# Kernel optimization log

Hardware: AMD Instinct MI355X
Metric: run time of the kernel (lower is better)

Reference implementation:

```python
import jax, jax.numpy as jnp
import numpy as np

N, E, D, R = 8192, 131072, 128, 32
SIZES = (3, 5, 7)  # per-degree component counts (2l+1)
LN_EPS = 1e-5


def setup_inputs() -> dict:
    key = jax.random.key(0)
    ks = jax.random.split(key, 20)
    rn = lambda k, shape, s=1.0: jax.random.normal(k, shape, jnp.float32) * s
    inp = {
        'X0': rn(ks[0], (N, SIZES[0], D)),
        'X1': rn(ks[1], (N, SIZES[1], D)),
        'X2': rn(ks[2], (N, SIZES[2], D)),
        't_ij': rn(ks[3], (E, D)),
        'r0': rn(ks[4], (E, SIZES[0])),
        'r1': rn(ks[5], (E, SIZES[1])),
        'r2': rn(ks[6], (E, SIZES[2])),
        'edge_index': jax.random.randint(ks[7], (2, E), 0, N, dtype=jnp.int32),
        # params
        'W_vq': rn(ks[8], (D, R), D ** -0.5),
        'W_vk0': rn(ks[9], (D, R), D ** -0.5),
        'W_vk1': rn(ks[10], (D, R), D ** -0.5),
        'W_vk2': rn(ks[11], (D, R), D ** -0.5),
        'ln_g': jnp.ones((R,), jnp.float32),
        'ln_b': jnp.zeros((R,), jnp.float32),
        'W_w': rn(ks[12], (R, D), R ** -0.5),
        'b_w': jnp.zeros((D,), jnp.float32),
        'W_t1': rn(ks[13], (D, D), D ** -0.5),
        'b_t1': jnp.zeros((D,), jnp.float32),
        'W_t2': rn(ks[14], (D, D), D ** -0.5),
        'b_t2': jnp.zeros((D,), jnp.float32),
    }
    return inp


def _vec_rej(x, r):
    # x: [E, L, R], r: [E, L]; dot over component dim (L), keepdim, subtract projection
    r = r[..., None]
    dot = jnp.sum(x * r, axis=1, keepdims=True)  # [E, 1, R]
    return x - dot * r


def reference(X0, X1, X2, t_ij, r0, r1, r2, edge_index,
              W_vq, W_vk0, W_vk1, W_vk2, ln_g, ln_b, W_w, b_w,
              W_t1, b_t1, W_t2, b_t2):
    n_j, n_i = edge_index[0], edge_index[1]
    X_ls = jnp.concatenate([X0, X1, X2], axis=1)                 # [N, 15, D]
    eq_i = jnp.einsum('nld,dr->nlr', X_ls, W_vq)[n_i]            # [E, 15, R]
    ek = jnp.concatenate([
        jnp.einsum('nld,dr->nlr', X0, W_vk0),
        jnp.einsum('nld,dr->nlr', X1, W_vk1),
        jnp.einsum('nld,dr->nlr', X2, W_vk2)], axis=1)
    ek_j = ek[n_j]                                               # [E, 15, R]
    # per-degree vector rejection (vec_rej=True)
    qs, ksl, off = [], [], 0
    for r in (r0, r1, r2):
        s = r.shape[1]
        qs.append(_vec_rej(eq_i[:, off:off + s], r))
        ksl.append(_vec_rej(ek_j[:, off:off + s], -r))
        off += s
    eq_i = jnp.concatenate(qs, axis=1)
    ek_j = jnp.concatenate(ksl, axis=1)
    w_ij = jnp.sum(eq_i * ek_j, axis=1)                          # [E, R]
    # mlp_w = LayerNorm + Linear
    mu = jnp.mean(w_ij, axis=-1, keepdims=True)
    var = jnp.var(w_ij, axis=-1, keepdims=True)
    wn = (w_ij - mu) * jax.lax.rsqrt(var + LN_EPS) * ln_g + ln_b
    dw = wn @ W_w + b_w                                          # [E, D]
    # mlp_t = Linear -> silu -> Linear, then outer activation
    t = jax.nn.silu(t_ij @ W_t1 + b_t1) @ W_t2 + b_t2            # [E, D]
    return dw * jax.nn.silu(t)
```

## Files before the change

### kernel.cpp

```cpp
#include <hip/hip_runtime.h>
#include <hip/hip_bf16.h>

#define N_NODES 8192
#define N_EDGES 131072
#define LN_EPS  1e-5f

typedef __attribute__((ext_vector_type(8))) short bf16x8;
typedef __attribute__((ext_vector_type(4))) float f32x4;

__device__ __forceinline__ float silu_f(float x) {
    return x / (1.0f + __expf(-x));
}

__device__ __forceinline__ unsigned short f2bf(float x) {
    union { float f; unsigned int u; } v; v.f = x;
    unsigned int r = v.u + 0x7FFFu + ((v.u >> 16) & 1u);
    return (unsigned short)(r >> 16);
}
__device__ __forceinline__ float bf2f(unsigned short u) {
    union { float f; unsigned int x; } v; v.x = ((unsigned int)u) << 16;
    return v.f;
}
__device__ __forceinline__ unsigned int pk2(float a, float b) {
    float2 t; t.x = a; t.y = b;
    union { __hip_bfloat162 h; unsigned int u; } v;
    v.h = __float22bfloat162_rn(t);
    return v.u;
}
__device__ __forceinline__ bf16x8 pack8(float4 u, float4 v) {
    union { bf16x8 b; unsigned int w[4]; } o;
    o.w[0] = pk2(u.x, u.y); o.w[1] = pk2(u.z, u.w);
    o.w[2] = pk2(v.x, v.y); o.w[3] = pk2(v.z, v.w);
    return o.b;
}
__device__ __forceinline__ f32x4 mfma16(bf16x8 a, bf16x8 b, f32x4 c) {
    return __builtin_amdgcn_mfma_f32_16x16x32_bf16(a, b, c, 0, 0, 0);
}

__global__ __launch_bounds__(256) void prep_kernel(
    const float* __restrict__ W_w, const float* __restrict__ W_t1,
    const float* __restrict__ W_t2, const float* __restrict__ Wvq,
    const float* __restrict__ Wvk0, const float* __restrict__ Wvk1,
    const float* __restrict__ Wvk2,
    unsigned short* __restrict__ Wtw, unsigned short* __restrict__ Wt1b,
    unsigned short* __restrict__ Wt2b, unsigned short* __restrict__ Wqt,
    unsigned short* __restrict__ Wk0t, unsigned short* __restrict__ Wk1t,
    unsigned short* __restrict__ Wk2t)
{
    int i = blockIdx.x * 256 + threadIdx.x;
    if (i < 16384) {
        int n = i >> 7, k = i & 127;
        Wt1b[i] = f2bf(W_t1[k * 128 + n]);
        Wt2b[i] = f2bf(W_t2[k * 128 + n]);
    }
    if (i < 4096) {
        { int n = i >> 5, k = i & 31; Wtw[i] = f2bf(W_w[k * 128 + n]); }
        int r = i >> 7, d = i & 127;
        Wqt[i]  = f2bf(Wvq [d * 32 + r]);
        Wk0t[i] = f2bf(Wvk0[d * 32 + r]);
        Wk1t[i] = f2bf(Wvk1[d * 32 + r]);
        Wk2t[i] = f2bf(Wvk2[d * 32 + r]);
    }
}

template<int S, int LOFF>
__device__ __forceinline__ void proj_body(
    const float* __restrict__ X, const unsigned short* __restrict__ Wqt,
    const unsigned short* __restrict__ Wkt,
    unsigned short* __restrict__ eq, unsigned short* __restrict__ ek,
    int row0)
{
    const int tid  = threadIdx.x;
    const int lane = tid & 63;
    const int wv   = tid >> 6;
    const int l15  = lane & 15;
    const int lk   = lane >> 4;
    const int xrow = row0 + wv * 16 + l15;

    bf16x8 xf[4];
    #pragma unroll
    for (int kt = 0; kt < 4; ++kt) {
        const float* p = X + (size_t)xrow * 128 + kt * 32 + lk * 8;
        xf[kt] = pack8(*(const float4*)p, *(const float4*)(p + 4));
    }

    f32x4 qa[2], ka[2];
    #pragma unroll
    for (int h = 0; h < 2; ++h) {
        qa[h] = (f32x4){0.f, 0.f, 0.f, 0.f};
        ka[h] = (f32x4){0.f, 0.f, 0.f, 0.f};
    }
    #pragma unroll
    for (int kt = 0; kt < 4; ++kt) {
        #pragma unroll
        for (int h = 0; h < 2; ++h) {
            bf16x8 wq = *(const bf16x8*)&Wqt[(h * 16 + l15) * 128 + kt * 32 + lk * 8];
            bf16x8 wk = *(const bf16x8*)&Wkt[(h * 16 + l15) * 128 + kt * 32 + lk * 8];
            qa[h] = mfma16(wq, xf[kt], qa[h]);
            ka[h] = mfma16(wk, xf[kt], ka[h]);
        }
    }

    const int n = xrow / S;
    const int l = xrow % S + LOFF;
    const size_t base = (size_t)n * 480 + (size_t)l * 32;
    #pragma unroll
    for (int h = 0; h < 2; ++h) {
        int rb = h * 16 + lk * 4;
        union { ushort4 s; unsigned int u[2]; } pq, pk_;
        pq.u[0]  = pk2(qa[h][0], qa[h][1]); pq.u[1]  = pk2(qa[h][2], qa[h][3]);
        pk_.u[0] = pk2(ka[h][0], ka[h][1]); pk_.u[1] = pk2(ka[h][2], ka[h][3]);
        *(ushort4*)&eq[base + rb] = pq.s;
        *(ushort4*)&ek[base + rb] = pk_.s;
    }
}

__global__ __launch_bounds__(256) void proj_kernel(
    const float* __restrict__ X0, const float* __restrict__ X1,
    const float* __restrict__ X2,
    const unsigned short* __restrict__ Wqt,
    const unsigned short* __restrict__ Wk0t,
    const unsigned short* __restrict__ Wk1t,
    const unsigned short* __restrict__ Wk2t,
    unsigned short* __restrict__ eq, unsigned short* __restrict__ ek)
{
    const int b = blockIdx.x;
    if (b < 384)
        proj_body<3, 0>(X0, Wqt, Wk0t, eq, ek, b * 64);
    else if (b < 1024)
        proj_body<5, 3>(X1, Wqt, Wk1t, eq, ek, (b - 384) * 64);
    else
        proj_body<7, 8>(X2, Wqt, Wk2t, eq, ek, (b - 1024) * 64);
}

__global__ __launch_bounds__(256) void wn_kernel(
    const unsigned short* __restrict__ eq, const unsigned short* __restrict__ ek,
    const float* __restrict__ r0, const float* __restrict__ r1,
    const float* __restrict__ r2, const int* __restrict__ eidx,
    const float* __restrict__ ln_g, const float* __restrict__ ln_b,
    unsigned short* __restrict__ wn)
{
    const int tid = threadIdx.x;
    const int r   = tid & 31;
    const int e   = blockIdx.x * 8 + (tid >> 5);
    const float g  = ln_g[r];
    const float bb = ln_b[r];
    const int nj = eidx[e];
    const int ni = eidx[N_EDGES + e];

    float q[15], k[15], rv[15];
    const unsigned short* qp = eq + (size_t)ni * 480 + r;
    const unsigned short* kp = ek + (size_t)nj * 480 + r;
    #pragma unroll
    for (int l = 0; l < 15; ++l) { q[l] = bf2f(qp[l * 32]); k[l] = bf2f(kp[l * 32]); }
    #pragma unroll
    for (int c = 0; c < 3; ++c) rv[c]     = r0[e * 3 + c];
    #pragma unroll
    for (int c = 0; c < 5; ++c) rv[3 + c] = r1[e * 5 + c];
    #pragma unroll
    for (int c = 0; c < 7; ++c) rv[8 + c] = r2[e * 7 + c];

    float dq, dk;
    dq = q[0]*rv[0] + q[1]*rv[1] + q[2]*rv[2];
    dk = k[0]*rv[0] + k[1]*rv[1] + k[2]*rv[2];
    #pragma unroll
    for (int l = 0; l < 3; ++l) { q[l] -= dq * rv[l]; k[l] -= dk * rv[l]; }
    dq = 0.f; dk = 0.f;
    #pragma unroll
    for (int l = 3; l < 8; ++l) { dq += q[l]*rv[l]; dk += k[l]*rv[l]; }
    #pragma unroll
    for (int l = 3; l < 8; ++l) { q[l] -= dq * rv[l]; k[l] -= dk * rv[l]; }
    dq = 0.f; dk = 0.f;
    #pragma unroll
    for (int l = 8; l < 15; ++l) { dq += q[l]*rv[l]; dk += k[l]*rv[l]; }
    #pragma unroll
    for (int l = 8; l < 15; ++l) { q[l] -= dq * rv[l]; k[l] -= dk * rv[l]; }

    float w = 0.f;
    #pragma unroll
    for (int l = 0; l < 15; ++l) w = fmaf(q[l], k[l], w);

    float s = w, s2 = w * w;
    s += __shfl_xor(s, 1);  s2 += __shfl_xor(s2, 1);
    s += __shfl_xor(s, 2);  s2 += __shfl_xor(s2, 2);
    s += __shfl_xor(s, 4);  s2 += __shfl_xor(s2, 4);
    s += __shfl_xor(s, 8);  s2 += __shfl_xor(s2, 8);
    s += __shfl_xor(s, 16); s2 += __shfl_xor(s2, 16);
    const float mu  = s * (1.f / 32.f);
    const float var = s2 * (1.f / 32.f) - mu * mu;
    const float wnv = (w - mu) * rsqrtf(var + LN_EPS) * g + bb;
    wn[(size_t)e * 32 + r] = f2bf(wnv);
}

__global__ __launch_bounds__(256) void edge_kernel(
    const float* __restrict__ t_ij,
    const unsigned short* __restrict__ wn,
    const unsigned short* __restrict__ Wtw, const float* __restrict__ b_w,
    const unsigned short* __restrict__ Wt1, const float* __restrict__ b_t1,
    const unsigned short* __restrict__ Wt2, const float* __restrict__ b_t2,
    float* __restrict__ out)
{
    __shared__ __align__(16) unsigned short Hp[4][32 * 128];

    const int tid  = threadIdx.x;
    const int lane = tid & 63;
    const int wv   = tid >> 6;
    const int l15  = lane & 15;
    const int lk   = lane >> 4;
    const int tile = (blockIdx.x * 4 + wv) * 32;
    char* hp = (char*)&Hp[wv][0];

    bf16x8 a1[4][2];
    #pragma unroll
    for (int kt = 0; kt < 4; ++kt)
        #pragma unroll
        for (int rt = 0; rt < 2; ++rt) {
            const float* p = t_ij + (size_t)(tile + rt * 16 + l15) * 128
                           + kt * 32 + lk * 8;
            a1[kt][rt] = pack8(*(const float4*)p, *(const float4*)(p + 4));
        }

    bf16x8 wnf[2];
    #pragma unroll
    for (int rt = 0; rt < 2; ++rt)
        wnf[rt] = *(const bf16x8*)&wn[(size_t)(tile + rt * 16 + l15) * 32 + lk * 8];

    #pragma unroll
    for (int ct = 0; ct < 8; ++ct) {
        bf16x8 w1f[4];
        #pragma unroll
        for (int kt = 0; kt < 4; ++kt)
            w1f[kt] = *(const bf16x8*)&Wt1[(size_t)(ct * 16 + l15) * 128
                                           + kt * 32 + lk * 8];
        f32x4 ac0 = (f32x4){0.f, 0.f, 0.f, 0.f};
        f32x4 ac1 = (f32x4){0.f, 0.f, 0.f, 0.f};
        #pragma unroll
        for (int kt = 0; kt < 4; ++kt) {
            ac0 = mfma16(a1[kt][0], w1f[kt], ac0);
            ac1 = mfma16(a1[kt][1], w1f[kt], ac1);
        }
        const float bb = b_t1[ct * 16 + l15];
        const int   n  = ct * 16 + l15;
        #pragma unroll
        for (int r = 0; r < 4; ++r) {
            int m0 = lk * 4 + r;
            int m1 = 16 + lk * 4 + r;
            *(unsigned short*)(hp + (((m0 * 128 + n) * 2) ^ ((m0 & 7) << 4)))
                = f2bf(silu_f(ac0[r] + bb));
            *(unsigned short*)(hp + (((m1 * 128 + n) * 2) ^ ((m1 & 7) << 4)))
                = f2bf(silu_f(ac1[r] + bb));
        }
    }

    bf16x8 a2[4][2];
    #pragma unroll
    for (int kt = 0; kt < 4; ++kt)
        #pragma unroll
        for (int rt = 0; rt < 2; ++rt) {
            int m2 = rt * 16 + l15;
            a2[kt][rt] = *(const bf16x8*)(hp +
                (((m2 * 128 + kt * 32 + lk * 8) * 2) ^ ((m2 & 7) << 4)));
        }

    #pragma unroll
    for (int ct = 0; ct < 8; ++ct) {
        bf16x8 w2f[4];
        #pragma unroll
        for (int kt = 0; kt < 4; ++kt)
            w2f[kt] = *(const bf16x8*)&Wt2[(size_t)(ct * 16 + l15) * 128
                                           + kt * 32 + lk * 8];
        bf16x8 wwf = *(const bf16x8*)&Wtw[(ct * 16 + l15) * 32 + lk * 8];

        f32x4 o0 = (f32x4){0.f, 0.f, 0.f, 0.f};
        f32x4 o1 = (f32x4){0.f, 0.f, 0.f, 0.f};
        #pragma unroll
        for (int kt = 0; kt < 4; ++kt) {
            o0 = mfma16(a2[kt][0], w2f[kt], o0);
            o1 = mfma16(a2[kt][1], w2f[kt], o1);
        }
        f32x4 d0 = mfma16(wnf[0], wwf, (f32x4){0.f, 0.f, 0.f, 0.f});
        f32x4 d1 = mfma16(wnf[1], wwf, (f32x4){0.f, 0.f, 0.f, 0.f});

        const float bwv = b_w[ct * 16 + l15];
        const float b2v = b_t2[ct * 16 + l15];
        const int   n   = ct * 16 + l15;
        #pragma unroll
        for (int r = 0; r < 4; ++r) {
            out[(size_t)(tile + lk * 4 + r) * 128 + n]
                = (d0[r] + bwv) * silu_f(o0[r] + b2v);
            out[(size_t)(tile + 16 + lk * 4 + r) * 128 + n]
                = (d1[r] + bwv) * silu_f(o1[r] + b2v);
        }
    }
}

extern "C" void kernel_launch(void* const* d_in, const int* in_sizes, int n_in,
                              void* d_out, int out_size, void* d_ws, size_t ws_size,
                              hipStream_t stream) {
    (void)in_sizes; (void)n_in; (void)out_size; (void)ws_size;
    const float* X0   = (const float*)d_in[0];
    const float* X1   = (const float*)d_in[1];
    const float* X2   = (const float*)d_in[2];
    const float* t_ij = (const float*)d_in[3];
    const float* r0   = (const float*)d_in[4];
    const float* r1   = (const float*)d_in[5];
    const float* r2   = (const float*)d_in[6];
    const int*   eidx = (const int*)d_in[7];
    const float* Wvq  = (const float*)d_in[8];
    const float* Wvk0 = (const float*)d_in[9];
    const float* Wvk1 = (const float*)d_in[10];
    const float* Wvk2 = (const float*)d_in[11];
    const float* ln_g = (const float*)d_in[12];
    const float* ln_b = (const float*)d_in[13];
    const float* W_w  = (const float*)d_in[14];
    const float* b_w  = (const float*)d_in[15];
    const float* W_t1 = (const float*)d_in[16];
    const float* b_t1 = (const float*)d_in[17];
    const float* W_t2 = (const float*)d_in[18];
    const float* b_t2 = (const float*)d_in[19];
    float* out = (float*)d_out;

    unsigned short* eq   = (unsigned short*)d_ws;
    unsigned short* ek   = eq  + (size_t)N_NODES * 480;
    unsigned short* wn   = ek  + (size_t)N_NODES * 480;
    unsigned short* Wtw  = wn  + (size_t)N_EDGES * 32;
    unsigned short* Wt1b = Wtw  + 4096;
    unsigned short* Wt2b = Wt1b + 16384;
    unsigned short* Wqt  = Wt2b + 16384;
    unsigned short* Wk0t = Wqt  + 4096;
    unsigned short* Wk1t = Wk0t + 4096;
    unsigned short* Wk2t = Wk1t + 4096;

    prep_kernel<<<64, 256, 0, stream>>>(W_w, W_t1, W_t2, Wvq, Wvk0, Wvk1, Wvk2,
                                        Wtw, Wt1b, Wt2b, Wqt, Wk0t, Wk1t, Wk2t);
    proj_kernel<<<1920, 256, 0, stream>>>(X0, X1, X2, Wqt, Wk0t, Wk1t, Wk2t,
                                          eq, ek);
    wn_kernel<<<N_EDGES / 8, 256, 0, stream>>>(eq, ek, r0, r1, r2, eidx,
                                               ln_g, ln_b, wn);
    edge_kernel<<<N_EDGES / 128, 256, 0, stream>>>(t_ij, wn, Wtw, b_w,
                                                   Wt1b, b_t1, Wt2b, b_t2, out);
}
```

Before: 114.5 us.

## Transpose eq/ek layout, widen edge tile to 64 rows, vectorize stores

Stores the projected q/k per node as [R][16] (padded from 15 components), so each wn thread reads its 15 components with two 16-byte loads instead of 15 strided scalar loads. The edge kernel now processes 64 edges per wave instead of 32. It swaps the MFMA operand order so each lane holds 4 consecutive output columns, which allows packed LDS writes and float4 global stores for the output. SiLU uses a hardware reciprocal instead of a division. The costs are more registers and LDS per wave, fewer blocks in flight, and scattered 2-byte stores in the projection kernel.

Result: faster. 110.1 us (-3.8%).

```diff
diff --git a/kernel.cpp b/kernel.cpp
--- a/kernel.cpp
+++ b/kernel.cpp
@@ -9,7 +9,7 @@
 typedef __attribute__((ext_vector_type(4))) float f32x4;
 
 __device__ __forceinline__ float silu_f(float x) {
-    return x / (1.0f + __expf(-x));
+    return x * __builtin_amdgcn_rcpf(1.0f + __expf(-x));
 }
 
 __device__ __forceinline__ unsigned short f2bf(float x) {
@@ -103,15 +103,15 @@
 
     const int n = xrow / S;
     const int l = xrow % S + LOFF;
-    const size_t base = (size_t)n * 480 + (size_t)l * 32;
+    const size_t base = (size_t)n * 512 + l;
     #pragma unroll
     for (int h = 0; h < 2; ++h) {
-        int rb = h * 16 + lk * 4;
-        union { ushort4 s; unsigned int u[2]; } pq, pk_;
-        pq.u[0]  = pk2(qa[h][0], qa[h][1]); pq.u[1]  = pk2(qa[h][2], qa[h][3]);
-        pk_.u[0] = pk2(ka[h][0], ka[h][1]); pk_.u[1] = pk2(ka[h][2], ka[h][3]);
-        *(ushort4*)&eq[base + rb] = pq.s;
-        *(ushort4*)&ek[base + rb] = pk_.s;
+        #pragma unroll
+        for (int j = 0; j < 4; ++j) {
+            const int r = h * 16 + lk * 4 + j;
+            eq[base + r * 16] = f2bf(qa[h][j]);
+            ek[base + r * 16] = f2bf(ka[h][j]);
+        }
     }
 }
 
@@ -148,11 +148,24 @@
     const int nj = eidx[e];
     const int ni = eidx[N_EDGES + e];
 
+    const unsigned short* qp = eq + (size_t)ni * 512 + r * 16;
+    const unsigned short* kp = ek + (size_t)nj * 512 + r * 16;
+    bf16x8 q0 = *(const bf16x8*)qp;
+    bf16x8 q1 = *(const bf16x8*)(qp + 8);
+    bf16x8 k0 = *(const bf16x8*)kp;
+    bf16x8 k1 = *(const bf16x8*)(kp + 8);
+
     float q[15], k[15], rv[15];
-    const unsigned short* qp = eq + (size_t)ni * 480 + r;
-    const unsigned short* kp = ek + (size_t)nj * 480 + r;
-    #pragma unroll
-    for (int l = 0; l < 15; ++l) { q[l] = bf2f(qp[l * 32]); k[l] = bf2f(kp[l * 32]); }
+    #pragma unroll
+    for (int l = 0; l < 8; ++l) {
+        q[l] = bf2f((unsigned short)q0[l]);
+        k[l] = bf2f((unsigned short)k0[l]);
+    }
+    #pragma unroll
+    for (int l = 8; l < 15; ++l) {
+        q[l] = bf2f((unsigned short)q1[l - 8]);
+        k[l] = bf2f((unsigned short)k1[l - 8]);
+    }
     #pragma unroll
     for (int c = 0; c < 3; ++c) rv[c]     = r0[e * 3 + c];
     #pragma unroll
@@ -200,29 +213,30 @@
     const unsigned short* __restrict__ Wt2, const float* __restrict__ b_t2,
     float* __restrict__ out)
 {
-    __shared__ __align__(16) unsigned short Hp[4][32 * 128];
+    __shared__ __align__(16) unsigned short Hp[4][64 * 128];
 
     const int tid  = threadIdx.x;
     const int lane = tid & 63;
     const int wv   = tid >> 6;
     const int l15  = lane & 15;
     const int lk   = lane >> 4;
-    const int tile = (blockIdx.x * 4 + wv) * 32;
+    const int tile = (blockIdx.x * 4 + wv) * 64;
     char* hp = (char*)&Hp[wv][0];
-
-    bf16x8 a1[4][2];
+    const int swz = (l15 & 7) << 4;
+
+    bf16x8 a1[4][4];
     #pragma unroll
     for (int kt = 0; kt < 4; ++kt)
         #pragma unroll
-        for (int rt = 0; rt < 2; ++rt) {
+        for (int rt = 0; rt < 4; ++rt) {
             const float* p = t_ij + (size_t)(tile + rt * 16 + l15) * 128
                            + kt * 32 + lk * 8;
             a1[kt][rt] = pack8(*(const float4*)p, *(const float4*)(p + 4));
         }
 
-    bf16x8 wnf[2];
-    #pragma unroll
-    for (int rt = 0; rt < 2; ++rt)
+    bf16x8 wnf[4];
+    #pragma unroll
+    for (int rt = 0; rt < 4; ++rt)
         wnf[rt] = *(const bf16x8*)&wn[(size_t)(tile + rt * 16 + l15) * 32 + lk * 8];
 
     #pragma unroll
@@ -232,35 +246,32 @@
         for (int kt = 0; kt < 4; ++kt)
             w1f[kt] = *(const bf16x8*)&Wt1[(size_t)(ct * 16 + l15) * 128
                                            + kt * 32 + lk * 8];
-        f32x4 ac0 = (f32x4){0.f, 0.f, 0.f, 0.f};
-        f32x4 ac1 = (f32x4){0.f, 0.f, 0.f, 0.f};
-        #pragma unroll
-        for (int kt = 0; kt < 4; ++kt) {
-            ac0 = mfma16(a1[kt][0], w1f[kt], ac0);
-            ac1 = mfma16(a1[kt][1], w1f[kt], ac1);
-        }
-        const float bb = b_t1[ct * 16 + l15];
-        const int   n  = ct * 16 + l15;
-        #pragma unroll
-        for (int r = 0; r < 4; ++r) {
-            int m0 = lk * 4 + r;
-            int m1 = 16 + lk * 4 + r;
-            *(unsigned short*)(hp + (((m0 * 128 + n) * 2) ^ ((m0 & 7) << 4)))
-                = f2bf(silu_f(ac0[r] + bb));
-            *(unsigned short*)(hp + (((m1 * 128 + n) * 2) ^ ((m1 & 7) << 4)))
-                = f2bf(silu_f(ac1[r] + bb));
-        }
-    }
-
-    bf16x8 a2[4][2];
+        f32x4 ac[4];
+        #pragma unroll
+        for (int rt = 0; rt < 4; ++rt) ac[rt] = (f32x4){0.f, 0.f, 0.f, 0.f};
+        #pragma unroll
+        for (int kt = 0; kt < 4; ++kt)
+            #pragma unroll
+            for (int rt = 0; rt < 4; ++rt)
+                ac[rt] = mfma16(w1f[kt], a1[kt][rt], ac[rt]);
+
+        const float4 bt1 = *(const float4*)&b_t1[ct * 16 + lk * 4];
+        #pragma unroll
+        for (int rt = 0; rt < 4; ++rt) {
+            uint2 hh;
+            hh.x = pk2(silu_f(ac[rt][0] + bt1.x), silu_f(ac[rt][1] + bt1.y));
+            hh.y = pk2(silu_f(ac[rt][2] + bt1.z), silu_f(ac[rt][3] + bt1.w));
+            *(uint2*)(hp + (((rt * 16 + l15) * 256 + ct * 32 + lk * 8) ^ swz)) = hh;
+        }
+    }
+
+    bf16x8 a2[4][4];
     #pragma unroll
     for (int kt = 0; kt < 4; ++kt)
         #pragma unroll
-        for (int rt = 0; rt < 2; ++rt) {
-            int m2 = rt * 16 + l15;
+        for (int rt = 0; rt < 4; ++rt)
             a2[kt][rt] = *(const bf16x8*)(hp +
-                (((m2 * 128 + kt * 32 + lk * 8) * 2) ^ ((m2 & 7) << 4)));
-        }
+                (((rt * 16 + l15) * 256 + kt * 64 + lk * 16) ^ swz));
 
     #pragma unroll
     for (int ct = 0; ct < 8; ++ct) {
@@ -271,25 +282,28 @@
                                            + kt * 32 + lk * 8];
         bf16x8 wwf = *(const bf16x8*)&Wtw[(ct * 16 + l15) * 32 + lk * 8];
 
-        f32x4 o0 = (f32x4){0.f, 0.f, 0.f, 0.f};
-        f32x4 o1 = (f32x4){0.f, 0.f, 0.f, 0.f};
-        #pragma unroll
-        for (int kt = 0; kt < 4; ++kt) {
-            o0 = mfma16(a2[kt][0], w2f[kt], o0);
-            o1 = mfma16(a2[kt][1], w2f[kt], o1);
-        }
-        f32x4 d0 = mfma16(wnf[0], wwf, (f32x4){0.f, 0.f, 0.f, 0.f});
-        f32x4 d1 = mfma16(wnf[1], wwf, (f32x4){0.f, 0.f, 0.f, 0.f});
-
-        const float bwv = b_w[ct * 16 + l15];
-        const float b2v = b_t2[ct * 16 + l15];
-        const int   n   = ct * 16 + l15;
-        #pragma unroll
-        for (int r = 0; r < 4; ++r) {
-            out[(size_t)(tile + lk * 4 + r) * 128 + n]
-                = (d0[r] + bwv) * silu_f(o0[r] + b2v);
-            out[(size_t)(tile + 16 + lk * 4 + r) * 128 + n]
-                = (d1[r] + bwv) * silu_f(o1[r] + b2v);
+        f32x4 o[4], d[4];
+        #pragma unroll
+        for (int rt = 0; rt < 4; ++rt) o[rt] = (f32x4){0.f, 0.f, 0.f, 0.f};
+        #pragma unroll
+        for (int kt = 0; kt < 4; ++kt)
+            #pragma unroll
+            for (int rt = 0; rt < 4; ++rt)
+                o[rt] = mfma16(w2f[kt], a2[kt][rt], o[rt]);
+        #pragma unroll
+        for (int rt = 0; rt < 4; ++rt)
+            d[rt] = mfma16(wwf, wnf[rt], (f32x4){0.f, 0.f, 0.f, 0.f});
+
+        const float4 bwv = *(const float4*)&b_w[ct * 16 + lk * 4];
+        const float4 b2v = *(const float4*)&b_t2[ct * 16 + lk * 4];
+        #pragma unroll
+        for (int rt = 0; rt < 4; ++rt) {
+            float4 s;
+            s.x = (d[rt][0] + bwv.x) * silu_f(o[rt][0] + b2v.x);
+            s.y = (d[rt][1] + bwv.y) * silu_f(o[rt][1] + b2v.y);
+            s.z = (d[rt][2] + bwv.z) * silu_f(o[rt][2] + b2v.z);
+            s.w = (d[rt][3] + bwv.w) * silu_f(o[rt][3] + b2v.w);
+            *(float4*)&out[(size_t)(tile + rt * 16 + l15) * 128 + ct * 16 + lk * 4] = s;
         }
     }
 }
@@ -321,8 +335,8 @@
     float* out = (float*)d_out;
 
     unsigned short* eq   = (unsigned short*)d_ws;
-    unsigned short* ek   = eq  + (size_t)N_NODES * 480;
-    unsigned short* wn   = ek  + (size_t)N_NODES * 480;
+    unsigned short* ek   = eq  + (size_t)N_NODES * 512;
+    unsigned short* wn   = ek  + (size_t)N_NODES * 512;
     unsigned short* Wtw  = wn  + (size_t)N_EDGES * 32;
     unsigned short* Wt1b = Wtw  + 4096;
     unsigned short* Wt2b = Wt1b + 16384;
@@ -337,6 +351,6 @@
                                           eq, ek);
     wn_kernel<<<N_EDGES / 8, 256, 0, stream>>>(eq, ek, r0, r1, r2, eidx,
                                                ln_g, ln_b, wn);
-    edge_kernel<<<N_EDGES / 128, 256, 0, stream>>>(t_ij, wn, Wtw, b_w,
+    edge_kernel<<<N_EDGES / 256, 256, 0, stream>>>(t_ij, wn, Wtw, b_w,
                                                    Wt1b, b_t1, Wt2b, b_t2, out);
 }
```
